# Kernel tuning notes

Measured on AMD Instinct MI355X. Metric: run time of the kernel, lower is better.

## Reference

```python
import jax, jax.numpy as jnp
import numpy as np

N_NODES = 50000
IN_DIM = 256
HID = 128
OUT_DIM = 64
N_LAYERS = 3
N_EDGES = 800000
BATCH = 4096
BN_EPS = 1e-5
LRELU_SLOPE = 0.01


def setup_inputs() -> dict:
    key = jax.random.key(0)
    ks = jax.random.split(key, 24)
    inp = {}
    inp["x"] = jax.random.normal(ks[0], (N_NODES, IN_DIM), jnp.float32)
    inp["edge_index"] = jax.random.randint(ks[1], (2, N_EDGES), 0, N_NODES, dtype=jnp.int32)
    inp["drug_pos_ids"] = jax.random.randint(ks[2], (BATCH,), 0, N_NODES, dtype=jnp.int32)
    inp["target_pos_ids"] = jax.random.randint(ks[3], (BATCH,), 0, N_NODES, dtype=jnp.int32)
    inp["drug_neg_ids"] = jax.random.randint(ks[4], (BATCH,), 0, N_NODES, dtype=jnp.int32)
    inp["target_neg_ids"] = jax.random.randint(ks[5], (BATCH,), 0, N_NODES, dtype=jnp.int32)
    inp["adjacency_matrix"] = jnp.zeros((1, 1), jnp.float32)  # dead arg in original forward
    # GCN layer params (xavier-normal-ish scale, zero bias as in __init__)
    for i in range(N_LAYERS):
        din = IN_DIM if i == 0 else HID
        inp[f"gcn_w{i}"] = jax.random.normal(ks[6 + i], (HID, din), jnp.float32) * np.float32(np.sqrt(2.0 / (din + HID)))
        inp[f"gcn_b{i}"] = jnp.zeros((HID,), jnp.float32)
    inp["bn_gamma"] = jnp.ones((HID,), jnp.float32)
    inp["bn_beta"] = jnp.zeros((HID,), jnp.float32)
    inp["W_D"] = jax.random.normal(ks[10], (HID, HID), jnp.float32) * np.float32(np.sqrt(2.0 / HID))
    inp["W_T"] = jax.random.normal(ks[11], (HID, HID), jnp.float32) * np.float32(np.sqrt(2.0 / HID))
    inp["q_D"] = jax.random.normal(ks[12], (HID,), jnp.float32)
    inp["q_T"] = jax.random.normal(ks[13], (HID,), jnp.float32)
    inp["out_w"] = jax.random.normal(ks[14], (OUT_DIM, HID), jnp.float32) * np.float32(np.sqrt(1.0 / HID))
    inp["out_b"] = jnp.zeros((OUT_DIM,), jnp.float32)
    return inp


def gcn_conv(x, w, b, src, dst, num_nodes):
    # PyG GCNConv: h = x @ W^T, then symmetric-normalized aggregation with self-loops
    h = x @ w.T                                           # [N, HID]
    deg = 1.0 + jax.ops.segment_sum(jnp.ones(src.shape[0], h.dtype), dst, num_segments=num_nodes)
    dinv = jax.lax.rsqrt(deg)                             # [N]
    norm = dinv[src] * dinv[dst]                          # [E]
    agg = jax.ops.segment_sum(h[src] * norm[:, None], dst, num_segments=num_nodes)
    agg = agg + h * (dinv * dinv)[:, None]                # self-loop contribution
    return agg + b


def batchnorm(x, gamma, beta):
    # training-mode BatchNorm1d math (batch statistics, biased var)
    mean = jnp.mean(x, axis=0)
    var = jnp.mean(jnp.square(x - mean), axis=0)
    return (x - mean) * jax.lax.rsqrt(var + BN_EPS) * gamma + beta


def attention_pooling(emb, W, q):
    # emb: [L, N, H]; softmax over the layer axis L
    h = jax.nn.leaky_relu(jnp.einsum('lnh,kh->lnk', emb, W), negative_slope=LRELU_SLOPE)
    e = jnp.einsum('lnk,k->ln', h, q)                     # [L, N]
    alpha = jax.nn.softmax(e, axis=0)
    return jnp.einsum('lnh,ln->nh', emb, alpha)           # [N, H]


def reference(x, edge_index, drug_pos_ids, target_pos_ids, drug_neg_ids, target_neg_ids,
              adjacency_matrix, gcn_w0, gcn_b0, gcn_w1, gcn_b1, gcn_w2, gcn_b2,
              bn_gamma, bn_beta, W_D, W_T, q_D, q_T, out_w, out_b):
    src, dst = edge_index[0], edge_index[1]
    num_nodes = x.shape[0]
    gcn_params = [(gcn_w0, gcn_b0), (gcn_w1, gcn_b1), (gcn_w2, gcn_b2)]
    layer_embs = []
    h = x
    for w, b in gcn_params:
        h = jax.nn.relu(gcn_conv(h, w, b, src, dst, num_nodes))
        h = batchnorm(h, bn_gamma, bn_beta)
        # dropout: identity (eval mode)
        layer_embs.append(h)
    emb = jnp.stack(layer_embs, axis=0)                   # [L, N, H]
    z_D = attention_pooling(emb, W_D, q_D) @ out_w.T + out_b
    z_T = attention_pooling(emb, W_T, q_T) @ out_w.T + out_b
    return (z_D[drug_pos_ids], z_T[target_pos_ids], z_D[drug_neg_ids], z_T[target_neg_ids])
```

## Files before the change

### kernel.cpp

```cpp
#include <hip/hip_runtime.h>
#include <hip/hip_fp16.h>
#include <cstdint>

#define N_NODES 50000
#define IN_DIM  256
#define HID     128
#define OUT_DIM 64
#define N_EDGES 800000
#define BATCH   4096
#define BN_EPS  1e-5f
#define SLOPE   0.01f

typedef unsigned short u16;
typedef __attribute__((ext_vector_type(8))) short bf16x8;
typedef __attribute__((ext_vector_type(4))) float f32x4;

__device__ __forceinline__ u16 f2bf(float f) {
    union { float f; unsigned u; } v; v.f = f;
    unsigned r = v.u + 0x7FFF + ((v.u >> 16) & 1);
    return (u16)(r >> 16);
}
__device__ __forceinline__ float bf2f(u16 b) {
    union { unsigned u; float f; } v; v.u = ((unsigned)b) << 16;
    return v.f;
}
__device__ __forceinline__ void splitbf(float v, u16* hi, u16* lo) {
    u16 h = f2bf(v);
    *hi = h;
    *lo = f2bf(v - bf2f(h));
}

__device__ __forceinline__ void swz_store(u16* __restrict__ buf, int K, int n, int k, float v) {
    int KC = K >> 7;
    int chunk = (n >> 6) * KC + (k >> 7);
    int base = chunk * 16384 + ((n >> 4) & 3) * 2048 + ((k >> 5) & 3) * 512
             + (((k >> 3) & 3) * 16 + (n & 15)) * 8 + (k & 7);
    u16 hi, lo;
    splitbf(v, &hi, &lo);
    buf[base] = hi;
    buf[base + 8192] = lo;
}

#define BNP_SPREAD 64
#define BNACC_PER_LAYER (BNP_SPREAD * 256)


#define PW0 (HID * IN_DIM)
#define PW1 (PW0 + HID * HID)
#define PW2 (PW1 + HID * HID)
#define PWD (PW2 + HID * HID)
#define PWT (PWD + HID * HID)
#define POW (PWT + OUT_DIM * HID)
#define PBN (POW + 3 * BNACC_PER_LAYER)
#define PBC (PBN + 256)
#define PTOT (PBC + 2 * 3 * 2 * BATCH)

__global__ void prep(const float* __restrict__ w0, const float* __restrict__ w1,
                     const float* __restrict__ w2, const float* __restrict__ WD,
                     const float* __restrict__ WT, const float* __restrict__ out_w,
                     u16* __restrict__ w0swz, u16* __restrict__ w1swz, u16* __restrict__ w2swz,
                     u16* __restrict__ wDTswz,
                     float* __restrict__ wt, float* __restrict__ bnacc3,
                     int* __restrict__ bucketCnt, float* __restrict__ ebuf) {
    int i = blockIdx.x * 256 + threadIdx.x;
    if (i < PW0) {
        swz_store(w0swz, IN_DIM, i >> 8, i & 255, w0[i]);
    } else if (i < PW1) {
        int j = i - PW0; swz_store(w1swz, HID, j >> 7, j & 127, w1[j]);
    } else if (i < PW2) {
        int j = i - PW1; swz_store(w2swz, HID, j >> 7, j & 127, w2[j]);
    } else if (i < PWD) {
        int j = i - PW2; swz_store(wDTswz, HID, j >> 7, j & 127, WD[j]);
    } else if (i < PWT) {
        int j = i - PWD; swz_store(wDTswz + 32768, HID, j >> 7, j & 127, WT[j]);
    } else if (i < POW) {
        int j = i - PWT;
        wt[j] = out_w[(j & 63) * HID + (j >> 6)];
    } else if (i < PBN) {
        bnacc3[i - POW] = 0.f;
    } else if (i < PBC) {
        bucketCnt[i - PBN] = 0;
    } else if (i < PTOT) {
        ebuf[i - PBC] = 0.f;
    }
}


#define NBKT 196
#define PASSA_CHUNK 2048
#define NB_A ((N_EDGES + PASSA_CHUNK - 1) / PASSA_CHUNK)

__global__ void bucket_count(const int* __restrict__ dst, int* __restrict__ bucketCnt) {
    __shared__ int hist[NBKT];
    int t = threadIdx.x;
    if (t < NBKT) hist[t] = 0;
    __syncthreads();
    int b0 = blockIdx.x * PASSA_CHUNK;
    int b1 = min(b0 + PASSA_CHUNK, N_EDGES);
    for (int i = b0 + t; i < b1; i += 256)
        atomicAdd(&hist[dst[i] >> 8], 1);
    __syncthreads();
    if (t < NBKT && hist[t] > 0) atomicAdd(&bucketCnt[t], hist[t]);
}

__global__ void bucket_scan(const int* __restrict__ bucketCnt, int* __restrict__ bucketBase,
                            int* __restrict__ gcursor, int* __restrict__ rowstart) {
    __shared__ int s[256];
    int t = threadIdx.x;
    int v = (t < NBKT) ? bucketCnt[t] : 0;
    s[t] = v;
    __syncthreads();
#pragma unroll
    for (int off = 1; off < 256; off <<= 1) {
        int tmp = (t >= off) ? s[t - off] : 0;
        __syncthreads();
        s[t] += tmp;
        __syncthreads();
    }
    if (t < NBKT) { bucketBase[t] = s[t] - v; gcursor[t] = s[t] - v; }
    if (t == 0) { bucketBase[NBKT] = N_EDGES; rowstart[N_NODES] = N_EDGES; }
}

__global__ void bucket_scatter(const int* __restrict__ src, const int* __restrict__ dst,
                               int* __restrict__ gcursor, unsigned* __restrict__ pairs) {
    __shared__ int hist[NBKT], base[NBKT], hist2[NBKT];
    int t = threadIdx.x;
    if (t < NBKT) { hist[t] = 0; hist2[t] = 0; }
    __syncthreads();
    int b0 = blockIdx.x * PASSA_CHUNK;
    int b1 = min(b0 + PASSA_CHUNK, N_EDGES);
    for (int i = b0 + t; i < b1; i += 256)
        atomicAdd(&hist[dst[i] >> 8], 1);
    __syncthreads();
    if (t < NBKT && hist[t] > 0) base[t] = atomicAdd(&gcursor[t], hist[t]);
    __syncthreads();
    for (int i = b0 + t; i < b1; i += 256) {
        int d = dst[i];
        int b = d >> 8;
        int lp = atomicAdd(&hist2[b], 1);
        pairs[base[b] + lp] = ((unsigned)(d & 255) << 16) | (unsigned)src[i];
    }
}

__global__ void bucket_build(const unsigned* __restrict__ pairs, const int* __restrict__ bucketBase,
                             int* __restrict__ rowstart, float* __restrict__ dinv,
                             int* __restrict__ csr) {
    __shared__ int cnt[256], s[256], lcur[256];
    int b = blockIdx.x, t = threadIdx.x;
    int pb0 = bucketBase[b], pb1 = bucketBase[b + 1];
    cnt[t] = 0;
    __syncthreads();
    for (int i = pb0 + t; i < pb1; i += 256)
        atomicAdd(&cnt[pairs[i] >> 16], 1);
    __syncthreads();
    int v = cnt[t];
    s[t] = v;
    __syncthreads();
#pragma unroll
    for (int off = 1; off < 256; off <<= 1) {
        int tmp = (t >= off) ? s[t - off] : 0;
        __syncthreads();
        s[t] += tmp;
        __syncthreads();
    }
    int node = (b << 8) + t;
    int start = pb0 + s[t] - v;
    if (node < N_NODES) {
        rowstart[node] = start;
        dinv[node] = rsqrtf(1.0f + (float)v);
    }
    lcur[t] = start;
    __syncthreads();
    for (int i = pb0 + t; i < pb1; i += 256) {
        unsigned pr = pairs[i];
        int pos = atomicAdd(&lcur[pr >> 16], 1);
        csr[pos] = (int)(pr & 0xFFFFu);
    }
}

__global__ void csr_pack(int* __restrict__ csr, const float* __restrict__ dinv) {
    int e = blockIdx.x * 256 + threadIdx.x;
    if (e < N_EDGES) {
        int sc = csr[e];
        __half hd = __float2half(dinv[sc]);
        csr[e] = ((int)*(u16*)&hd << 16) | sc;
    }
}


__global__ __launch_bounds__(256) void gemm_tile(const float* __restrict__ A,
                                                 const float* __restrict__ bnss,
                                                 const u16* __restrict__ Bswz,
                                                 u16* __restrict__ Cout,
                                                 int M, int K) {
    __shared__ u16 Bs[32768];
    const int tid  = threadIdx.x;
    const int wave = tid >> 6, lane = tid & 63;
    const int lr   = lane & 15, quad = lane >> 4;
    const int rowBase = blockIdx.x * 64;
    const int KC = K >> 7;

    f32x4 acc[8];
#pragma unroll
    for (int c = 0; c < 8; ++c) acc[c] = (f32x4){0.f, 0.f, 0.f, 0.f};

    const int arow = rowBase + wave * 16 + lr;
    const bool rv = arow < M;

    for (int kc = 0; kc < KC; ++kc) {
        if (kc) __syncthreads();
        const uint4* s0 = (const uint4*)(Bswz + (size_t)kc * 16384);
        const uint4* s1 = (const uint4*)(Bswz + (size_t)(KC + kc) * 16384);
        uint4* B4 = (uint4*)Bs;
#pragma unroll
        for (int i = 0; i < 8; ++i)
            B4[i * 256 + tid] = s0[i * 256 + tid];
#pragma unroll
        for (int i = 0; i < 8; ++i)
            B4[2048 + i * 256 + tid] = s1[i * 256 + tid];
        __syncthreads();

#pragma unroll
        for (int kkidx = 0; kkidx < 4; ++kkidx) {
            const int kcol = kc * 128 + kkidx * 32 + quad * 8;
            float av[8];
            if (rv) {
                const float* ap = A + (size_t)arow * K + kcol;
                float4 v0 = ((const float4*)ap)[0];
                float4 v1 = ((const float4*)ap)[1];
                av[0] = v0.x; av[1] = v0.y; av[2] = v0.z; av[3] = v0.w;
                av[4] = v1.x; av[5] = v1.y; av[6] = v1.z; av[7] = v1.w;
            } else {
#pragma unroll
                for (int j = 0; j < 8; ++j) av[j] = 0.f;
            }
            if (bnss) {
#pragma unroll
                for (int j = 0; j < 8; ++j) {
                    float sc = bnss[kcol + j];
                    float sh = bnss[K + kcol + j];
                    av[j] = fmaf(av[j], sc, sh);
                }
            }
            bf16x8 ah, al;
#pragma unroll
            for (int j = 0; j < 8; ++j) {
                u16 hi, lo;
                splitbf(av[j], &hi, &lo);
                ((u16*)&ah)[j] = hi; ((u16*)&al)[j] = lo;
            }
#pragma unroll
            for (int c = 0; c < 8; ++c) {
                const int lb = (c >> 2) * 16384 + (c & 3) * 2048 + kkidx * 512 + lane * 8;
                bf16x8 bh = *(const bf16x8*)&Bs[lb];
                bf16x8 bl = *(const bf16x8*)&Bs[lb + 8192];
                acc[c] = __builtin_amdgcn_mfma_f32_16x16x32_bf16(al, bh, acc[c], 0, 0, 0);
                acc[c] = __builtin_amdgcn_mfma_f32_16x16x32_bf16(ah, bl, acc[c], 0, 0, 0);
                acc[c] = __builtin_amdgcn_mfma_f32_16x16x32_bf16(ah, bh, acc[c], 0, 0, 0);
            }
        }
    }

    const int rowb = rowBase + wave * 16 + quad * 4;
#pragma unroll
    for (int reg = 0; reg < 4; ++reg) {
        int row = rowb + reg;
        if (row < M) {
#pragma unroll
            for (int c = 0; c < 8; ++c) {
                int col = c * 16 + lr;
                __half hv = __float2half(acc[c][reg]);
                Cout[(size_t)row * 128 + col] = *(u16*)&hv;
            }
        }
    }
}


__global__ __launch_bounds__(256) void pool_gemm(const float* __restrict__ emb0,
                                                 const float* __restrict__ emb1,
                                                 const float* __restrict__ emb2,
                                                 const float* __restrict__ bnss3,
                                                 const int* __restrict__ dpos, const int* __restrict__ dneg,
                                                 const int* __restrict__ tpos, const int* __restrict__ tneg,
                                                 const u16* __restrict__ wDTswz,
                                                 const float* __restrict__ q_D, const float* __restrict__ q_T,
                                                 float* __restrict__ e_D, float* __restrict__ e_T) {
    __shared__ u16 Bs[32768];
    const int head = blockIdx.y;
    const u16* Bswz = wDTswz + head * 32768;
    const float* q  = head ? q_T : q_D;
    float* eo = head ? e_T : e_D;
    const int* ia = head ? tpos : dpos;
    const int* ib = head ? tneg : dneg;

    const int tid  = threadIdx.x;
    const int wave = tid >> 6, lane = tid & 63;
    const int lr   = lane & 15, quad = lane >> 4;
    const int rowBase = blockIdx.x * 64;

    const int arow = rowBase + wave * 16 + lr;
    const int l0 = arow >> 13, j0 = arow & 8191;
    const int node0 = (j0 < BATCH) ? ia[j0] : ib[j0 - BATCH];
    const float* embs[3] = {emb0, emb1, emb2};
    const float* A0 = embs[l0] + (size_t)node0 * HID;
    const float* bn0 = bnss3 + l0 * 2 * HID;

    f32x4 acc[8];
#pragma unroll
    for (int c = 0; c < 8; ++c) acc[c] = (f32x4){0.f, 0.f, 0.f, 0.f};

    uint4* B4 = (uint4*)Bs;
    const uint4* srcB = (const uint4*)Bswz;
#pragma unroll
    for (int i = 0; i < 16; ++i)
        B4[i * 256 + tid] = srcB[i * 256 + tid];
    __syncthreads();

#pragma unroll
    for (int kkidx = 0; kkidx < 4; ++kkidx) {
        const int kcol = kkidx * 32 + quad * 8;
        float av[8];
        {
            float4 v0 = ((const float4*)(A0 + kcol))[0];
            float4 v1 = ((const float4*)(A0 + kcol))[1];
            av[0] = v0.x; av[1] = v0.y; av[2] = v0.z; av[3] = v0.w;
            av[4] = v1.x; av[5] = v1.y; av[6] = v1.z; av[7] = v1.w;
        }
#pragma unroll
        for (int j = 0; j < 8; ++j)
            av[j] = fmaf(av[j], bn0[kcol + j], bn0[HID + kcol + j]);
        bf16x8 ah, al;
#pragma unroll
        for (int j = 0; j < 8; ++j) {
            u16 hi, lo;
            splitbf(av[j], &hi, &lo);
            ((u16*)&ah)[j] = hi; ((u16*)&al)[j] = lo;
        }
#pragma unroll
        for (int c = 0; c < 8; ++c) {
            const int lb = (c >> 2) * 16384 + (c & 3) * 2048 + kkidx * 512 + lane * 8;
            bf16x8 bh = *(const bf16x8*)&Bs[lb];
            bf16x8 bl = *(const bf16x8*)&Bs[lb + 8192];
            acc[c] = __builtin_amdgcn_mfma_f32_16x16x32_bf16(al, bh, acc[c], 0, 0, 0);
            acc[c] = __builtin_amdgcn_mfma_f32_16x16x32_bf16(ah, bl, acc[c], 0, 0, 0);
            acc[c] = __builtin_amdgcn_mfma_f32_16x16x32_bf16(ah, bh, acc[c], 0, 0, 0);
        }
    }

    float qv[8];
#pragma unroll
    for (int c = 0; c < 8; ++c) qv[c] = q[c * 16 + lr];
    const int rowb = rowBase + wave * 16 + quad * 4;
#pragma unroll
    for (int reg = 0; reg < 4; ++reg) {
        float p = 0.f;
#pragma unroll
        for (int c = 0; c < 8; ++c) {
            float v = acc[c][reg];
            v = (v > 0.f) ? v : SLOPE * v;
            p = fmaf(v, qv[c], p);
        }
        p += __shfl_xor(p, 1);
        p += __shfl_xor(p, 2);
        p += __shfl_xor(p, 4);
        p += __shfl_xor(p, 8);
        if (lr == 0) eo[rowb + reg] = p;
    }
}


__global__ __launch_bounds__(256) void agg_relu(const u16* __restrict__ h,
                                                const float* __restrict__ dinv,
                                                const int* __restrict__ rowstart,
                                                const int* __restrict__ csr,
                                                const float* __restrict__ bias,
                                                float* __restrict__ out,
                                                float* __restrict__ bnpart) {
    __shared__ float s_s[HID], s_sq[HID];
    int tid  = threadIdx.x;
    int wave = tid >> 6;
    int lane = tid & 63;
    int ep = lane >> 5;
    int q  = lane & 31;
    if (tid < HID) { s_s[tid] = 0.f; s_sq[tid] = 0.f; }
    __syncthreads();

    float bs0 = 0.f, bs1 = 0.f, bs2 = 0.f, bs3 = 0.f;
    float bq0 = 0.f, bq1 = 0.f, bq2 = 0.f, bq3 = 0.f;

#pragma unroll
    for (int it = 0; it < 4; ++it) {
        int n = blockIdx.x * 16 + wave * 4 + it;
        if (n < N_NODES) {
            int s = rowstart[n], e1 = rowstart[n + 1];
            float ax = 0.f, ay = 0.f, az = 0.f, aw = 0.f;
            int e = s + ep;
            for (; e + 6 < e1; e += 8) {
                unsigned c0 = (unsigned)csr[e];
                unsigned c1 = (unsigned)csr[e + 2];
                unsigned c2 = (unsigned)csr[e + 4];
                unsigned c3 = (unsigned)csr[e + 6];
                u16 d0 = (u16)(c0 >> 16), d1 = (u16)(c1 >> 16), d2 = (u16)(c2 >> 16), d3 = (u16)(c3 >> 16);
                float dv0 = __half2float(*(const __half*)&d0);
                float dv1 = __half2float(*(const __half*)&d1);
                float dv2 = __half2float(*(const __half*)&d2);
                float dv3 = __half2float(*(const __half*)&d3);
                uint2 w0 = ((const uint2*)(h + (size_t)(c0 & 0xFFFFu) * HID))[q];
                uint2 w1 = ((const uint2*)(h + (size_t)(c1 & 0xFFFFu) * HID))[q];
                uint2 w2 = ((const uint2*)(h + (size_t)(c2 & 0xFFFFu) * HID))[q];
                uint2 w3 = ((const uint2*)(h + (size_t)(c3 & 0xFFFFu) * HID))[q];
                float2 a0 = __half22float2(*(const __half2*)&w0.x), b0 = __half22float2(*(const __half2*)&w0.y);
                float2 a1 = __half22float2(*(const __half2*)&w1.x), b1 = __half22float2(*(const __half2*)&w1.y);
                float2 a2 = __half22float2(*(const __half2*)&w2.x), b2 = __half22float2(*(const __half2*)&w2.y);
                float2 a3 = __half22float2(*(const __half2*)&w3.x), b3 = __half22float2(*(const __half2*)&w3.y);
                ax = fmaf(dv0, a0.x, ax); ay = fmaf(dv0, a0.y, ay); az = fmaf(dv0, b0.x, az); aw = fmaf(dv0, b0.y, aw);
                ax = fmaf(dv1, a1.x, ax); ay = fmaf(dv1, a1.y, ay); az = fmaf(dv1, b1.x, az); aw = fmaf(dv1, b1.y, aw);
                ax = fmaf(dv2, a2.x, ax); ay = fmaf(dv2, a2.y, ay); az = fmaf(dv2, b2.x, az); aw = fmaf(dv2, b2.y, aw);
                ax = fmaf(dv3, a3.x, ax); ay = fmaf(dv3, a3.y, ay); az = fmaf(dv3, b3.x, az); aw = fmaf(dv3, b3.y, aw);
            }
            for (; e < e1; e += 2) {
                unsigned c0 = (unsigned)csr[e];
                u16 d0 = (u16)(c0 >> 16);
                float dv = __half2float(*(const __half*)&d0);
                uint2 w0 = ((const uint2*)(h + (size_t)(c0 & 0xFFFFu) * HID))[q];
                float2 a0 = __half22float2(*(const __half2*)&w0.x);
                float2 b0 = __half22float2(*(const __half2*)&w0.y);
                ax = fmaf(dv, a0.x, ax); ay = fmaf(dv, a0.y, ay);
                az = fmaf(dv, b0.x, az); aw = fmaf(dv, b0.y, aw);
            }
            ax += __shfl_xor(ax, 32);
            ay += __shfl_xor(ay, 32);
            az += __shfl_xor(az, 32);
            aw += __shfl_xor(aw, 32);
            if (ep == 0) {
                float dn = dinv[n];
                float dn2 = dn * dn;
                uint2 hw = ((const uint2*)(h + (size_t)n * HID))[q];
                float2 h0 = __half22float2(*(const __half2*)&hw.x);
                float2 h1 = __half22float2(*(const __half2*)&hw.y);
                float4 bv = ((const float4*)bias)[q];
                float4 o;
                o.x = fmaxf(fmaf(ax, dn, fmaf(h0.x, dn2, bv.x)), 0.f);
                o.y = fmaxf(fmaf(ay, dn, fmaf(h0.y, dn2, bv.y)), 0.f);
                o.z = fmaxf(fmaf(az, dn, fmaf(h1.x, dn2, bv.z)), 0.f);
                o.w = fmaxf(fmaf(aw, dn, fmaf(h1.y, dn2, bv.w)), 0.f);
                ((float4*)(out + (size_t)n * HID))[q] = o;
                bs0 += o.x; bq0 = fmaf(o.x, o.x, bq0);
                bs1 += o.y; bq1 = fmaf(o.y, o.y, bq1);
                bs2 += o.z; bq2 = fmaf(o.z, o.z, bq2);
                bs3 += o.w; bq3 = fmaf(o.w, o.w, bq3);
            }
        }
    }

    if (ep == 0) {
        atomicAdd(&s_s[q * 4 + 0], bs0);
        atomicAdd(&s_s[q * 4 + 1], bs1);
        atomicAdd(&s_s[q * 4 + 2], bs2);
        atomicAdd(&s_s[q * 4 + 3], bs3);
        atomicAdd(&s_sq[q * 4 + 0], bq0);
        atomicAdd(&s_sq[q * 4 + 1], bq1);
        atomicAdd(&s_sq[q * 4 + 2], bq2);
        atomicAdd(&s_sq[q * 4 + 3], bq3);
    }
    __syncthreads();
    float* bp = bnpart + (size_t)(blockIdx.x & (BNP_SPREAD - 1)) * 256;
    if (tid < HID) atomicAdd(&bp[tid], s_s[tid]);
    else           atomicAdd(&bp[tid], s_sq[tid - HID]);
}

__global__ void bn_finalize(const float* __restrict__ acc,
                            const float* __restrict__ gamma, const float* __restrict__ beta,
                            float* __restrict__ bnss) {
    int f = threadIdx.x;
    float st = 0.f, sqt = 0.f;
    for (int p = 0; p < BNP_SPREAD; ++p) {
        st  += acc[p * 256 + f];
        sqt += acc[p * 256 + HID + f];
    }
    float mean = st * (1.0f / N_NODES);
    float var  = fmaxf(sqt * (1.0f / N_NODES) - mean * mean, 0.f);
    float sc   = gamma[f] * rsqrtf(var + BN_EPS);
    bnss[f] = sc;
    bnss[HID + f] = beta[f] - mean * sc;
}


__global__ void softmax_pool(const float* __restrict__ e0, const float* __restrict__ e1,
                             const float* __restrict__ e2, const float* __restrict__ bnss3,
                             const int* __restrict__ dpos, const int* __restrict__ dneg,
                             const int* __restrict__ tpos, const int* __restrict__ tneg,
                             const float* __restrict__ e_D, const float* __restrict__ e_T,
                             float* __restrict__ P_D, float* __restrict__ P_T) {
    int j = blockIdx.x;
    int f = threadIdx.x;
    int head = blockIdx.y;
    const int* ia = head ? tpos : dpos;
    const int* ib = head ? tneg : dneg;
    const float* e = head ? e_T : e_D;
    float* P = head ? P_T : P_D;
    int node = (j < BATCH) ? ia[j] : ib[j - BATCH];
    float l0 = e[j], l1 = e[2 * BATCH + j], l2 = e[4 * BATCH + j];
    float m = fmaxf(l0, fmaxf(l1, l2));
    float a0 = expf(l0 - m), a1 = expf(l1 - m), a2 = expf(l2 - m);
    float inv = 1.0f / (a0 + a1 + a2);
    float v0 = fmaf(e0[(size_t)node * HID + f], bnss3[f],           bnss3[HID + f]);
    float v1 = fmaf(e1[(size_t)node * HID + f], bnss3[2 * HID + f], bnss3[3 * HID + f]);
    float v2 = fmaf(e2[(size_t)node * HID + f], bnss3[4 * HID + f], bnss3[5 * HID + f]);
    P[(size_t)j * HID + f] = (a0 * v0 + a1 * v1 + a2 * v2) * inv;
}


__global__ __launch_bounds__(256) void head_gemm(const float* __restrict__ P_D,
                                                 const float* __restrict__ P_T,
                                                 const float* __restrict__ B,
                                                 const float* __restrict__ bias,
                                                 float* __restrict__ out) {
    constexpr int BM = 64, BK = 32, BN = OUT_DIM, TM = 4, TN = 4;
    __shared__ float As[BK][BM];
    __shared__ float Bs[BK][BN];
    const int y = blockIdx.y;
    const float* A = ((y & 1) ? P_T : P_D) + (size_t)(y >> 1) * BATCH * HID;
    float* C = out + (size_t)y * BATCH * OUT_DIM;
    const int tid = threadIdx.x;
    const int tx = tid & 15, ty = tid >> 4;
    const int rowBase = blockIdx.x * BM;
    float acc[TM][TN];
#pragma unroll
    for (int i = 0; i < TM; ++i)
#pragma unroll
        for (int j = 0; j < TN; ++j) acc[i][j] = 0.f;

    for (int kk = 0; kk < HID; kk += BK) {
#pragma unroll
        for (int i = tid; i < (BM * BK) / 4; i += 256) {
            int m  = i >> 3;
            int kq = i & 7;
            float4 v = *(const float4*)(A + (size_t)(rowBase + m) * HID + kk + kq * 4);
            As[kq * 4 + 0][m] = v.x;
            As[kq * 4 + 1][m] = v.y;
            As[kq * 4 + 2][m] = v.z;
            As[kq * 4 + 3][m] = v.w;
        }
#pragma unroll
        for (int i = tid; i < (BK * BN) / 4; i += 256) {
            int k  = i / (BN / 4);
            int n4 = i % (BN / 4);
            *(float4*)&Bs[k][n4 * 4] = *(const float4*)(B + (size_t)(kk + k) * BN + n4 * 4);
        }
        __syncthreads();
#pragma unroll 8
        for (int k = 0; k < BK; ++k) {
            float a[TM], b[TN];
#pragma unroll
            for (int i = 0; i < TM; ++i) a[i] = As[k][ty * TM + i];
#pragma unroll
            for (int j = 0; j < TN; ++j) b[j] = Bs[k][tx * TN + j];
#pragma unroll
            for (int i = 0; i < TM; ++i)
#pragma unroll
                for (int j = 0; j < TN; ++j)
                    acc[i][j] = fmaf(a[i], b[j], acc[i][j]);
        }
        __syncthreads();
    }
#pragma unroll
    for (int i = 0; i < TM; ++i) {
        int grow = rowBase + ty * TM + i;
#pragma unroll
        for (int j = 0; j < TN; ++j)
            C[(size_t)grow * BN + tx * TN + j] = acc[i][j] + bias[tx * TN + j];
    }
}


extern "C" void kernel_launch(void* const* d_in, const int* in_sizes, int n_in,
                              void* d_out, int out_size, void* d_ws, size_t ws_size,
                              hipStream_t stream) {
    const float* x          = (const float*)d_in[0];
    const int*   ei         = (const int*)d_in[1];
    const int*   srcp       = ei;
    const int*   dstp       = ei + N_EDGES;
    const int*   drug_pos   = (const int*)d_in[2];
    const int*   target_pos = (const int*)d_in[3];
    const int*   drug_neg   = (const int*)d_in[4];
    const int*   target_neg = (const int*)d_in[5];
    const float* gcn_w[3]   = {(const float*)d_in[7], (const float*)d_in[9], (const float*)d_in[11]};
    const float* gcn_b[3]   = {(const float*)d_in[8], (const float*)d_in[10], (const float*)d_in[12]};
    const float* gamma      = (const float*)d_in[13];
    const float* beta       = (const float*)d_in[14];
    const float* W_D        = (const float*)d_in[15];
    const float* W_T        = (const float*)d_in[16];
    const float* q_D        = (const float*)d_in[17];
    const float* q_T        = (const float*)d_in[18];
    const float* out_w      = (const float*)d_in[19];
    const float* out_b      = (const float*)d_in[20];
    float*       out        = (float*)d_out;

    char* p = (char*)d_ws;
    auto alloc = [&](size_t bytes) -> char* {
        char* r = p;
        p += (bytes + 255) & ~(size_t)255;
        return r;
    };
    char*  reg1  = alloc(sizeof(float) * (size_t)N_NODES * HID);
    float* emb0  = (float*)alloc(sizeof(float) * (size_t)N_NODES * HID);
    float* emb1  = (float*)alloc(sizeof(float) * (size_t)N_NODES * HID);
    float* emb2  = (float*)alloc(sizeof(float) * (size_t)N_NODES * HID);
    float* ebuf  = (float*)alloc(sizeof(float) * (size_t)2 * 3 * 2 * BATCH);
    u16*   w0swz = (u16*)alloc(sizeof(u16) * 2 * HID * IN_DIM);
    u16*   w1swz = (u16*)alloc(sizeof(u16) * 2 * HID * HID);
    u16*   w2swz = (u16*)alloc(sizeof(u16) * 2 * HID * HID);
    u16*   wDTswz = (u16*)alloc(sizeof(u16) * 4 * HID * HID);
    float* wt    = (float*)alloc(sizeof(float) * OUT_DIM * HID);
    int*   rowstart = (int*)alloc(sizeof(int) * (N_NODES + 1));
    int*   csr   = (int*)alloc(sizeof(int) * N_EDGES);
    unsigned* pairs = (unsigned*)alloc(sizeof(unsigned) * N_EDGES);
    float* dinvp = (float*)alloc(sizeof(float) * N_NODES);
    int*   bucketCnt  = (int*)alloc(sizeof(int) * 256);
    int*   bucketBase = (int*)alloc(sizeof(int) * (NBKT + 1));
    int*   gcursor    = (int*)alloc(sizeof(int) * 256);
    float* bnacc3 = (float*)alloc(sizeof(float) * 3 * BNACC_PER_LAYER);
    float* bnss3  = (float*)alloc(sizeof(float) * 3 * 2 * HID);
    if ((size_t)(p - (char*)d_ws) > ws_size) return;

    u16*   hbuf = (u16*)reg1;
    float* P_D  = (float*)reg1;
    float* P_T  = P_D + (size_t)2 * BATCH * HID;
    float* e_D  = ebuf;
    float* e_T  = ebuf + 3 * 2 * BATCH;
    float* embp[3] = {emb0, emb1, emb2};
    const u16* wswz[3] = {w0swz, w1swz, w2swz};

    prep<<<(PTOT + 255) / 256, 256, 0, stream>>>(
        gcn_w[0], gcn_w[1], gcn_w[2], W_D, W_T, out_w,
        w0swz, w1swz, w2swz, wDTswz, wt, bnacc3, bucketCnt, ebuf);

    bucket_count<<<NB_A, 256, 0, stream>>>(dstp, bucketCnt);
    bucket_scan<<<1, 256, 0, stream>>>(bucketCnt, bucketBase, gcursor, rowstart);
    bucket_scatter<<<NB_A, 256, 0, stream>>>(srcp, dstp, gcursor, pairs);
    bucket_build<<<NBKT, 256, 0, stream>>>(pairs, bucketBase, rowstart, dinvp, csr);
    csr_pack<<<(N_EDGES + 255) / 256, 256, 0, stream>>>(csr, dinvp);

    const int GB = (N_NODES + 63) / 64;
    for (int l = 0; l < 3; ++l) {
        int din = (l == 0) ? IN_DIM : HID;
        const float* Ain = (l == 0) ? x : embp[l - 1];
        const float* bnss = (l == 0) ? nullptr : (bnss3 + (l - 1) * 2 * HID);
        gemm_tile<<<GB, 256, 0, stream>>>(Ain, bnss, wswz[l], hbuf, N_NODES, din);
        agg_relu<<<(N_NODES + 15) / 16, 256, 0, stream>>>(hbuf, dinvp, rowstart, csr, gcn_b[l],
                                                          embp[l], bnacc3 + l * BNACC_PER_LAYER);
        bn_finalize<<<1, HID, 0, stream>>>(bnacc3 + l * BNACC_PER_LAYER, gamma, beta,
                                           bnss3 + l * 2 * HID);
    }

    const int RG = 3 * 2 * BATCH;
    pool_gemm<<<dim3(RG / 64, 2), 256, 0, stream>>>(
        emb0, emb1, emb2, bnss3, drug_pos, drug_neg, target_pos, target_neg,
        wDTswz, q_D, q_T, e_D, e_T);
    softmax_pool<<<dim3(2 * BATCH, 2), HID, 0, stream>>>(
        emb0, emb1, emb2, bnss3, drug_pos, drug_neg, target_pos, target_neg,
        e_D, e_T, P_D, P_T);

    head_gemm<<<dim3(BATCH / 64, 4), 256, 0, stream>>>(P_D, P_T, wt, out_b, out);
}
```

Before: 412.7 us.

## Map four nodes per wave with 16 lanes each using 16-byte row gathers

Result: faster. 403.9 us (-2.1%).

```diff
diff --git a/kernel.cpp b/kernel.cpp
--- a/kernel.cpp
+++ b/kernel.cpp
@@ -381,88 +381,130 @@
     int tid  = threadIdx.x;
     int wave = tid >> 6;
     int lane = tid & 63;
-    int ep = lane >> 5;
-    int q  = lane & 31;
+    int slot = lane >> 4;
+    int q    = lane & 15;
     if (tid < HID) { s_s[tid] = 0.f; s_sq[tid] = 0.f; }
     __syncthreads();
 
-    float bs0 = 0.f, bs1 = 0.f, bs2 = 0.f, bs3 = 0.f;
-    float bq0 = 0.f, bq1 = 0.f, bq2 = 0.f, bq3 = 0.f;
-
-#pragma unroll
-    for (int it = 0; it < 4; ++it) {
-        int n = blockIdx.x * 16 + wave * 4 + it;
-        if (n < N_NODES) {
-            int s = rowstart[n], e1 = rowstart[n + 1];
-            float ax = 0.f, ay = 0.f, az = 0.f, aw = 0.f;
-            int e = s + ep;
-            for (; e + 6 < e1; e += 8) {
-                unsigned c0 = (unsigned)csr[e];
-                unsigned c1 = (unsigned)csr[e + 2];
-                unsigned c2 = (unsigned)csr[e + 4];
-                unsigned c3 = (unsigned)csr[e + 6];
-                u16 d0 = (u16)(c0 >> 16), d1 = (u16)(c1 >> 16), d2 = (u16)(c2 >> 16), d3 = (u16)(c3 >> 16);
-                float dv0 = __half2float(*(const __half*)&d0);
-                float dv1 = __half2float(*(const __half*)&d1);
-                float dv2 = __half2float(*(const __half*)&d2);
-                float dv3 = __half2float(*(const __half*)&d3);
-                uint2 w0 = ((const uint2*)(h + (size_t)(c0 & 0xFFFFu) * HID))[q];
-                uint2 w1 = ((const uint2*)(h + (size_t)(c1 & 0xFFFFu) * HID))[q];
-                uint2 w2 = ((const uint2*)(h + (size_t)(c2 & 0xFFFFu) * HID))[q];
-                uint2 w3 = ((const uint2*)(h + (size_t)(c3 & 0xFFFFu) * HID))[q];
-                float2 a0 = __half22float2(*(const __half2*)&w0.x), b0 = __half22float2(*(const __half2*)&w0.y);
-                float2 a1 = __half22float2(*(const __half2*)&w1.x), b1 = __half22float2(*(const __half2*)&w1.y);
-                float2 a2 = __half22float2(*(const __half2*)&w2.x), b2 = __half22float2(*(const __half2*)&w2.y);
-                float2 a3 = __half22float2(*(const __half2*)&w3.x), b3 = __half22float2(*(const __half2*)&w3.y);
-                ax = fmaf(dv0, a0.x, ax); ay = fmaf(dv0, a0.y, ay); az = fmaf(dv0, b0.x, az); aw = fmaf(dv0, b0.y, aw);
-                ax = fmaf(dv1, a1.x, ax); ay = fmaf(dv1, a1.y, ay); az = fmaf(dv1, b1.x, az); aw = fmaf(dv1, b1.y, aw);
-                ax = fmaf(dv2, a2.x, ax); ay = fmaf(dv2, a2.y, ay); az = fmaf(dv2, b2.x, az); aw = fmaf(dv2, b2.y, aw);
-                ax = fmaf(dv3, a3.x, ax); ay = fmaf(dv3, a3.y, ay); az = fmaf(dv3, b3.x, az); aw = fmaf(dv3, b3.y, aw);
-            }
-            for (; e < e1; e += 2) {
-                unsigned c0 = (unsigned)csr[e];
-                u16 d0 = (u16)(c0 >> 16);
-                float dv = __half2float(*(const __half*)&d0);
-                uint2 w0 = ((const uint2*)(h + (size_t)(c0 & 0xFFFFu) * HID))[q];
-                float2 a0 = __half22float2(*(const __half2*)&w0.x);
-                float2 b0 = __half22float2(*(const __half2*)&w0.y);
-                ax = fmaf(dv, a0.x, ax); ay = fmaf(dv, a0.y, ay);
-                az = fmaf(dv, b0.x, az); aw = fmaf(dv, b0.y, aw);
-            }
-            ax += __shfl_xor(ax, 32);
-            ay += __shfl_xor(ay, 32);
-            az += __shfl_xor(az, 32);
-            aw += __shfl_xor(aw, 32);
-            if (ep == 0) {
-                float dn = dinv[n];
-                float dn2 = dn * dn;
-                uint2 hw = ((const uint2*)(h + (size_t)n * HID))[q];
-                float2 h0 = __half22float2(*(const __half2*)&hw.x);
-                float2 h1 = __half22float2(*(const __half2*)&hw.y);
-                float4 bv = ((const float4*)bias)[q];
-                float4 o;
-                o.x = fmaxf(fmaf(ax, dn, fmaf(h0.x, dn2, bv.x)), 0.f);
-                o.y = fmaxf(fmaf(ay, dn, fmaf(h0.y, dn2, bv.y)), 0.f);
-                o.z = fmaxf(fmaf(az, dn, fmaf(h1.x, dn2, bv.z)), 0.f);
-                o.w = fmaxf(fmaf(aw, dn, fmaf(h1.y, dn2, bv.w)), 0.f);
-                ((float4*)(out + (size_t)n * HID))[q] = o;
-                bs0 += o.x; bq0 = fmaf(o.x, o.x, bq0);
-                bs1 += o.y; bq1 = fmaf(o.y, o.y, bq1);
-                bs2 += o.z; bq2 = fmaf(o.z, o.z, bq2);
-                bs3 += o.w; bq3 = fmaf(o.w, o.w, bq3);
-            }
-        }
-    }
-
-    if (ep == 0) {
-        atomicAdd(&s_s[q * 4 + 0], bs0);
-        atomicAdd(&s_s[q * 4 + 1], bs1);
-        atomicAdd(&s_s[q * 4 + 2], bs2);
-        atomicAdd(&s_s[q * 4 + 3], bs3);
-        atomicAdd(&s_sq[q * 4 + 0], bq0);
-        atomicAdd(&s_sq[q * 4 + 1], bq1);
-        atomicAdd(&s_sq[q * 4 + 2], bq2);
-        atomicAdd(&s_sq[q * 4 + 3], bq3);
+    float bs[8], bq[8];
+#pragma unroll
+    for (int j = 0; j < 8; ++j) { bs[j] = 0.f; bq[j] = 0.f; }
+
+    int n = blockIdx.x * 16 + wave * 4 + slot;
+    if (n < N_NODES) {
+        int s = rowstart[n], e1 = rowstart[n + 1];
+        float a[8];
+#pragma unroll
+        for (int j = 0; j < 8; ++j) a[j] = 0.f;
+
+        int e = s;
+        for (; e + 3 < e1; e += 4) {
+            unsigned c0 = (unsigned)csr[e];
+            unsigned c1 = (unsigned)csr[e + 1];
+            unsigned c2 = (unsigned)csr[e + 2];
+            unsigned c3 = (unsigned)csr[e + 3];
+            u16 d0 = (u16)(c0 >> 16), d1 = (u16)(c1 >> 16), d2 = (u16)(c2 >> 16), d3 = (u16)(c3 >> 16);
+            float dv0 = __half2float(*(const __half*)&d0);
+            float dv1 = __half2float(*(const __half*)&d1);
+            float dv2 = __half2float(*(const __half*)&d2);
+            float dv3 = __half2float(*(const __half*)&d3);
+            uint4 w0 = ((const uint4*)(h + (size_t)(c0 & 0xFFFFu) * HID))[q];
+            uint4 w1 = ((const uint4*)(h + (size_t)(c1 & 0xFFFFu) * HID))[q];
+            uint4 w2 = ((const uint4*)(h + (size_t)(c2 & 0xFFFFu) * HID))[q];
+            uint4 w3 = ((const uint4*)(h + (size_t)(c3 & 0xFFFFu) * HID))[q];
+            {
+                float2 p0 = __half22float2(*(const __half2*)&w0.x);
+                float2 p1 = __half22float2(*(const __half2*)&w0.y);
+                float2 p2 = __half22float2(*(const __half2*)&w0.z);
+                float2 p3 = __half22float2(*(const __half2*)&w0.w);
+                a[0] = fmaf(dv0, p0.x, a[0]); a[1] = fmaf(dv0, p0.y, a[1]);
+                a[2] = fmaf(dv0, p1.x, a[2]); a[3] = fmaf(dv0, p1.y, a[3]);
+                a[4] = fmaf(dv0, p2.x, a[4]); a[5] = fmaf(dv0, p2.y, a[5]);
+                a[6] = fmaf(dv0, p3.x, a[6]); a[7] = fmaf(dv0, p3.y, a[7]);
+            }
+            {
+                float2 p0 = __half22float2(*(const __half2*)&w1.x);
+                float2 p1 = __half22float2(*(const __half2*)&w1.y);
+                float2 p2 = __half22float2(*(const __half2*)&w1.z);
+                float2 p3 = __half22float2(*(const __half2*)&w1.w);
+                a[0] = fmaf(dv1, p0.x, a[0]); a[1] = fmaf(dv1, p0.y, a[1]);
+                a[2] = fmaf(dv1, p1.x, a[2]); a[3] = fmaf(dv1, p1.y, a[3]);
+                a[4] = fmaf(dv1, p2.x, a[4]); a[5] = fmaf(dv1, p2.y, a[5]);
+                a[6] = fmaf(dv1, p3.x, a[6]); a[7] = fmaf(dv1, p3.y, a[7]);
+            }
+            {
+                float2 p0 = __half22float2(*(const __half2*)&w2.x);
+                float2 p1 = __half22float2(*(const __half2*)&w2.y);
+                float2 p2 = __half22float2(*(const __half2*)&w2.z);
+                float2 p3 = __half22float2(*(const __half2*)&w2.w);
+                a[0] = fmaf(dv2, p0.x, a[0]); a[1] = fmaf(dv2, p0.y, a[1]);
+                a[2] = fmaf(dv2, p1.x, a[2]); a[3] = fmaf(dv2, p1.y, a[3]);
+                a[4] = fmaf(dv2, p2.x, a[4]); a[5] = fmaf(dv2, p2.y, a[5]);
+                a[6] = fmaf(dv2, p3.x, a[6]); a[7] = fmaf(dv2, p3.y, a[7]);
+            }
+            {
+                float2 p0 = __half22float2(*(const __half2*)&w3.x);
+                float2 p1 = __half22float2(*(const __half2*)&w3.y);
+                float2 p2 = __half22float2(*(const __half2*)&w3.z);
+                float2 p3 = __half22float2(*(const __half2*)&w3.w);
+                a[0] = fmaf(dv3, p0.x, a[0]); a[1] = fmaf(dv3, p0.y, a[1]);
+                a[2] = fmaf(dv3, p1.x, a[2]); a[3] = fmaf(dv3, p1.y, a[3]);
+                a[4] = fmaf(dv3, p2.x, a[4]); a[5] = fmaf(dv3, p2.y, a[5]);
+                a[6] = fmaf(dv3, p3.x, a[6]); a[7] = fmaf(dv3, p3.y, a[7]);
+            }
+        }
+        for (; e < e1; ++e) {
+            unsigned c0 = (unsigned)csr[e];
+            u16 d0 = (u16)(c0 >> 16);
+            float dv0 = __half2float(*(const __half*)&d0);
+            uint4 w0 = ((const uint4*)(h + (size_t)(c0 & 0xFFFFu) * HID))[q];
+            float2 p0 = __half22float2(*(const __half2*)&w0.x);
+            float2 p1 = __half22float2(*(const __half2*)&w0.y);
+            float2 p2 = __half22float2(*(const __half2*)&w0.z);
+            float2 p3 = __half22float2(*(const __half2*)&w0.w);
+            a[0] = fmaf(dv0, p0.x, a[0]); a[1] = fmaf(dv0, p0.y, a[1]);
+            a[2] = fmaf(dv0, p1.x, a[2]); a[3] = fmaf(dv0, p1.y, a[3]);
+            a[4] = fmaf(dv0, p2.x, a[4]); a[5] = fmaf(dv0, p2.y, a[5]);
+            a[6] = fmaf(dv0, p3.x, a[6]); a[7] = fmaf(dv0, p3.y, a[7]);
+        }
+
+        float dn = dinv[n];
+        float dn2 = dn * dn;
+        uint4 hw = ((const uint4*)(h + (size_t)n * HID))[q];
+        float2 h0 = __half22float2(*(const __half2*)&hw.x);
+        float2 h1 = __half22float2(*(const __half2*)&hw.y);
+        float2 h2 = __half22float2(*(const __half2*)&hw.z);
+        float2 h3 = __half22float2(*(const __half2*)&hw.w);
+        float hv[8] = {h0.x, h0.y, h1.x, h1.y, h2.x, h2.y, h3.x, h3.y};
+        float4 bv0 = ((const float4*)bias)[2 * q];
+        float4 bv1 = ((const float4*)bias)[2 * q + 1];
+        float bb[8] = {bv0.x, bv0.y, bv0.z, bv0.w, bv1.x, bv1.y, bv1.z, bv1.w};
+        float o[8];
+#pragma unroll
+        for (int j = 0; j < 8; ++j) {
+            o[j] = fmaxf(fmaf(a[j], dn, fmaf(hv[j], dn2, bb[j])), 0.f);
+            bs[j] += o[j];
+            bq[j] = fmaf(o[j], o[j], bq[j]);
+        }
+        float4 o0 = {o[0], o[1], o[2], o[3]};
+        float4 o1 = {o[4], o[5], o[6], o[7]};
+        ((float4*)(out + (size_t)n * HID))[2 * q]     = o0;
+        ((float4*)(out + (size_t)n * HID))[2 * q + 1] = o1;
+    }
+
+#pragma unroll
+    for (int j = 0; j < 8; ++j) {
+        bs[j] += __shfl_xor(bs[j], 16);
+        bs[j] += __shfl_xor(bs[j], 32);
+        bq[j] += __shfl_xor(bq[j], 16);
+        bq[j] += __shfl_xor(bq[j], 32);
+    }
+    if (slot == 0) {
+#pragma unroll
+        for (int j = 0; j < 8; ++j) {
+            atomicAdd(&s_s[q * 8 + j], bs[j]);
+            atomicAdd(&s_sq[q * 8 + j], bq[j]);
+        }
     }
     __syncthreads();
     float* bp = bnpart + (size_t)(blockIdx.x & (BNP_SPREAD - 1)) * 256;
```

## Pre-scale GEMM rows by dinv, slice features into 32-wide blocks for aggregation

Applied to the files above, without the earlier changes.

Result: slower. 472.3 us (+14.4%).

```diff
diff --git a/kernel.cpp b/kernel.cpp
--- a/kernel.cpp
+++ b/kernel.cpp
@@ -144,7 +144,7 @@
 
 __global__ void bucket_build(const unsigned* __restrict__ pairs, const int* __restrict__ bucketBase,
                              int* __restrict__ rowstart, float* __restrict__ dinv,
-                             int* __restrict__ csr) {
+                             u16* __restrict__ csr) {
     __shared__ int cnt[256], s[256], lcur[256];
     int b = blockIdx.x, t = threadIdx.x;
     int pb0 = bucketBase[b], pb1 = bucketBase[b + 1];
@@ -174,16 +174,7 @@
     for (int i = pb0 + t; i < pb1; i += 256) {
         unsigned pr = pairs[i];
         int pos = atomicAdd(&lcur[pr >> 16], 1);
-        csr[pos] = (int)(pr & 0xFFFFu);
-    }
-}
-
-__global__ void csr_pack(int* __restrict__ csr, const float* __restrict__ dinv) {
-    int e = blockIdx.x * 256 + threadIdx.x;
-    if (e < N_EDGES) {
-        int sc = csr[e];
-        __half hd = __float2half(dinv[sc]);
-        csr[e] = ((int)*(u16*)&hd << 16) | sc;
+        csr[pos] = (u16)(pr & 0xFFFFu);
     }
 }
 
@@ -191,6 +182,7 @@
 __global__ __launch_bounds__(256) void gemm_tile(const float* __restrict__ A,
                                                  const float* __restrict__ bnss,
                                                  const u16* __restrict__ Bswz,
+                                                 const float* __restrict__ dinv,
                                                  u16* __restrict__ Cout,
                                                  int M, int K) {
     __shared__ u16 Bs[32768];
@@ -266,11 +258,13 @@
     for (int reg = 0; reg < 4; ++reg) {
         int row = rowb + reg;
         if (row < M) {
+            float dn = dinv[row];
 #pragma unroll
             for (int c = 0; c < 8; ++c) {
-                int col = c * 16 + lr;
-                __half hv = __float2half(acc[c][reg]);
-                Cout[(size_t)row * 128 + col] = *(u16*)&hv;
+                __half hv = __float2half(acc[c][reg] * dn);
+                u16* dst = Cout + (size_t)(c >> 1) * ((size_t)N_NODES * 32)
+                         + (size_t)row * 32 + (c & 1) * 16 + lr;
+                __builtin_nontemporal_store(*(u16*)&hv, dst);
             }
         }
     }
@@ -370,104 +364,79 @@
 }
 
 
-__global__ __launch_bounds__(256) void agg_relu(const u16* __restrict__ h,
-                                                const float* __restrict__ dinv,
-                                                const int* __restrict__ rowstart,
-                                                const int* __restrict__ csr,
-                                                const float* __restrict__ bias,
-                                                float* __restrict__ out,
-                                                float* __restrict__ bnpart) {
-    __shared__ float s_s[HID], s_sq[HID];
-    int tid  = threadIdx.x;
-    int wave = tid >> 6;
-    int lane = tid & 63;
-    int ep = lane >> 5;
-    int q  = lane & 31;
-    if (tid < HID) { s_s[tid] = 0.f; s_sq[tid] = 0.f; }
-    __syncthreads();
-
-    float bs0 = 0.f, bs1 = 0.f, bs2 = 0.f, bs3 = 0.f;
-    float bq0 = 0.f, bq1 = 0.f, bq2 = 0.f, bq3 = 0.f;
-
-#pragma unroll
-    for (int it = 0; it < 4; ++it) {
-        int n = blockIdx.x * 16 + wave * 4 + it;
-        if (n < N_NODES) {
-            int s = rowstart[n], e1 = rowstart[n + 1];
-            float ax = 0.f, ay = 0.f, az = 0.f, aw = 0.f;
-            int e = s + ep;
-            for (; e + 6 < e1; e += 8) {
-                unsigned c0 = (unsigned)csr[e];
-                unsigned c1 = (unsigned)csr[e + 2];
-                unsigned c2 = (unsigned)csr[e + 4];
-                unsigned c3 = (unsigned)csr[e + 6];
-                u16 d0 = (u16)(c0 >> 16), d1 = (u16)(c1 >> 16), d2 = (u16)(c2 >> 16), d3 = (u16)(c3 >> 16);
-                float dv0 = __half2float(*(const __half*)&d0);
-                float dv1 = __half2float(*(const __half*)&d1);
-                float dv2 = __half2float(*(const __half*)&d2);
-                float dv3 = __half2float(*(const __half*)&d3);
-                uint2 w0 = ((const uint2*)(h + (size_t)(c0 & 0xFFFFu) * HID))[q];
-                uint2 w1 = ((const uint2*)(h + (size_t)(c1 & 0xFFFFu) * HID))[q];
-                uint2 w2 = ((const uint2*)(h + (size_t)(c2 & 0xFFFFu) * HID))[q];
-                uint2 w3 = ((const uint2*)(h + (size_t)(c3 & 0xFFFFu) * HID))[q];
-                float2 a0 = __half22float2(*(const __half2*)&w0.x), b0 = __half22float2(*(const __half2*)&w0.y);
-                float2 a1 = __half22float2(*(const __half2*)&w1.x), b1 = __half22float2(*(const __half2*)&w1.y);
-                float2 a2 = __half22float2(*(const __half2*)&w2.x), b2 = __half22float2(*(const __half2*)&w2.y);
-                float2 a3 = __half22float2(*(const __half2*)&w3.x), b3 = __half22float2(*(const __half2*)&w3.y);
-                ax = fmaf(dv0, a0.x, ax); ay = fmaf(dv0, a0.y, ay); az = fmaf(dv0, b0.x, az); aw = fmaf(dv0, b0.y, aw);
-                ax = fmaf(dv1, a1.x, ax); ay = fmaf(dv1, a1.y, ay); az = fmaf(dv1, b1.x, az); aw = fmaf(dv1, b1.y, aw);
-                ax = fmaf(dv2, a2.x, ax); ay = fmaf(dv2, a2.y, ay); az = fmaf(dv2, b2.x, az); aw = fmaf(dv2, b2.y, aw);
-                ax = fmaf(dv3, a3.x, ax); ay = fmaf(dv3, a3.y, ay); az = fmaf(dv3, b3.x, az); aw = fmaf(dv3, b3.y, aw);
-            }
-            for (; e < e1; e += 2) {
-                unsigned c0 = (unsigned)csr[e];
-                u16 d0 = (u16)(c0 >> 16);
-                float dv = __half2float(*(const __half*)&d0);
-                uint2 w0 = ((const uint2*)(h + (size_t)(c0 & 0xFFFFu) * HID))[q];
-                float2 a0 = __half22float2(*(const __half2*)&w0.x);
-                float2 b0 = __half22float2(*(const __half2*)&w0.y);
-                ax = fmaf(dv, a0.x, ax); ay = fmaf(dv, a0.y, ay);
-                az = fmaf(dv, b0.x, az); aw = fmaf(dv, b0.y, aw);
-            }
-            ax += __shfl_xor(ax, 32);
-            ay += __shfl_xor(ay, 32);
-            az += __shfl_xor(az, 32);
-            aw += __shfl_xor(aw, 32);
-            if (ep == 0) {
-                float dn = dinv[n];
-                float dn2 = dn * dn;
-                uint2 hw = ((const uint2*)(h + (size_t)n * HID))[q];
-                float2 h0 = __half22float2(*(const __half2*)&hw.x);
-                float2 h1 = __half22float2(*(const __half2*)&hw.y);
-                float4 bv = ((const float4*)bias)[q];
-                float4 o;
-                o.x = fmaxf(fmaf(ax, dn, fmaf(h0.x, dn2, bv.x)), 0.f);
-                o.y = fmaxf(fmaf(ay, dn, fmaf(h0.y, dn2, bv.y)), 0.f);
-                o.z = fmaxf(fmaf(az, dn, fmaf(h1.x, dn2, bv.z)), 0.f);
-                o.w = fmaxf(fmaf(aw, dn, fmaf(h1.y, dn2, bv.w)), 0.f);
-                ((float4*)(out + (size_t)n * HID))[q] = o;
-                bs0 += o.x; bq0 = fmaf(o.x, o.x, bq0);
-                bs1 += o.y; bq1 = fmaf(o.y, o.y, bq1);
-                bs2 += o.z; bq2 = fmaf(o.z, o.z, bq2);
-                bs3 += o.w; bq3 = fmaf(o.w, o.w, bq3);
-            }
-        }
-    }
-
-    if (ep == 0) {
-        atomicAdd(&s_s[q * 4 + 0], bs0);
-        atomicAdd(&s_s[q * 4 + 1], bs1);
-        atomicAdd(&s_s[q * 4 + 2], bs2);
-        atomicAdd(&s_s[q * 4 + 3], bs3);
-        atomicAdd(&s_sq[q * 4 + 0], bq0);
-        atomicAdd(&s_sq[q * 4 + 1], bq1);
-        atomicAdd(&s_sq[q * 4 + 2], bq2);
-        atomicAdd(&s_sq[q * 4 + 3], bq3);
+#define AGG_NG ((N_NODES + 127) / 128)
+
+__global__ __launch_bounds__(256) void agg_slice(const u16* __restrict__ hblk,
+                                                 const float* __restrict__ dinv,
+                                                 const int* __restrict__ rowstart,
+                                                 const u16* __restrict__ csr,
+                                                 const float* __restrict__ bias,
+                                                 float* __restrict__ out,
+                                                 float* __restrict__ bnpart) {
+    __shared__ float s_s[32], s_sq[32];
+    const int tid  = threadIdx.x;
+    const int wave = tid >> 6, lane = tid & 63;
+    const int eg = lane >> 3;
+    const int q  = lane & 7;
+    const int x = blockIdx.x & 7;
+    const int slice = x >> 1, sub = x & 1;
+    const int g = blockIdx.x >> 3;
+    const u16* hs = hblk + (size_t)slice * ((size_t)N_NODES * 32);
+    if (tid < 32) { s_s[tid] = 0.f; s_sq[tid] = 0.f; }
+    __syncthreads();
+
+    float bsum[4] = {0.f, 0.f, 0.f, 0.f}, bsq[4] = {0.f, 0.f, 0.f, 0.f};
+    const int nbase = ((g * 2 + sub) * 4 + wave) * 16;
+    float4 bv = ((const float4*)(bias + slice * 32))[q];
+
+    for (int it = 0; it < 16; ++it) {
+        int n = nbase + it;
+        if (n >= N_NODES) break;
+        int s = rowstart[n], e1 = rowstart[n + 1];
+        float dn = dinv[n];
+        float a0 = 0.f, a1 = 0.f, a2 = 0.f, a3 = 0.f;
+#pragma unroll 2
+        for (int e = s + eg; e < e1; e += 8) {
+            int c = csr[e];
+            uint2 w = *(const uint2*)(hs + (size_t)c * 32 + q * 4);
+            float2 p0 = __half22float2(*(const __half2*)&w.x);
+            float2 p1 = __half22float2(*(const __half2*)&w.y);
+            a0 += p0.x; a1 += p0.y; a2 += p1.x; a3 += p1.y;
+        }
+        a0 += __shfl_xor(a0, 8);  a1 += __shfl_xor(a1, 8);
+        a2 += __shfl_xor(a2, 8);  a3 += __shfl_xor(a3, 8);
+        a0 += __shfl_xor(a0, 16); a1 += __shfl_xor(a1, 16);
+        a2 += __shfl_xor(a2, 16); a3 += __shfl_xor(a3, 16);
+        a0 += __shfl_xor(a0, 32); a1 += __shfl_xor(a1, 32);
+        a2 += __shfl_xor(a2, 32); a3 += __shfl_xor(a3, 32);
+        if (eg == 0) {
+            uint2 sw = *(const uint2*)(hs + (size_t)n * 32 + q * 4);
+            float2 s0 = __half22float2(*(const __half2*)&sw.x);
+            float2 s1 = __half22float2(*(const __half2*)&sw.y);
+            f32x4 o;
+            o.x = fmaxf(fmaf(dn, a0 + s0.x, bv.x), 0.f);
+            o.y = fmaxf(fmaf(dn, a1 + s0.y, bv.y), 0.f);
+            o.z = fmaxf(fmaf(dn, a2 + s1.x, bv.z), 0.f);
+            o.w = fmaxf(fmaf(dn, a3 + s1.y, bv.w), 0.f);
+            __builtin_nontemporal_store(o, (f32x4*)(out + (size_t)n * HID + slice * 32 + q * 4));
+            bsum[0] += o.x; bsq[0] = fmaf(o.x, o.x, bsq[0]);
+            bsum[1] += o.y; bsq[1] = fmaf(o.y, o.y, bsq[1]);
+            bsum[2] += o.z; bsq[2] = fmaf(o.z, o.z, bsq[2]);
+            bsum[3] += o.w; bsq[3] = fmaf(o.w, o.w, bsq[3]);
+        }
+    }
+
+    if (eg == 0) {
+#pragma unroll
+        for (int j = 0; j < 4; ++j) {
+            atomicAdd(&s_s[q * 4 + j], bsum[j]);
+            atomicAdd(&s_sq[q * 4 + j], bsq[j]);
+        }
     }
     __syncthreads();
     float* bp = bnpart + (size_t)(blockIdx.x & (BNP_SPREAD - 1)) * 256;
-    if (tid < HID) atomicAdd(&bp[tid], s_s[tid]);
-    else           atomicAdd(&bp[tid], s_sq[tid - HID]);
+    if (tid < 32)      atomicAdd(&bp[slice * 32 + tid], s_s[tid]);
+    else if (tid < 64) atomicAdd(&bp[128 + slice * 32 + (tid - 32)], s_sq[tid - 32]);
 }
 
 __global__ void bn_finalize(const float* __restrict__ acc,
@@ -615,7 +584,7 @@
     u16*   wDTswz = (u16*)alloc(sizeof(u16) * 4 * HID * HID);
     float* wt    = (float*)alloc(sizeof(float) * OUT_DIM * HID);
     int*   rowstart = (int*)alloc(sizeof(int) * (N_NODES + 1));
-    int*   csr   = (int*)alloc(sizeof(int) * N_EDGES);
+    u16*   csr   = (u16*)alloc(sizeof(int) * N_EDGES);
     unsigned* pairs = (unsigned*)alloc(sizeof(unsigned) * N_EDGES);
     float* dinvp = (float*)alloc(sizeof(float) * N_NODES);
     int*   bucketCnt  = (int*)alloc(sizeof(int) * 256);
@@ -641,16 +610,15 @@
     bucket_scan<<<1, 256, 0, stream>>>(bucketCnt, bucketBase, gcursor, rowstart);
     bucket_scatter<<<NB_A, 256, 0, stream>>>(srcp, dstp, gcursor, pairs);
     bucket_build<<<NBKT, 256, 0, stream>>>(pairs, bucketBase, rowstart, dinvp, csr);
-    csr_pack<<<(N_EDGES + 255) / 256, 256, 0, stream>>>(csr, dinvp);
 
     const int GB = (N_NODES + 63) / 64;
     for (int l = 0; l < 3; ++l) {
         int din = (l == 0) ? IN_DIM : HID;
         const float* Ain = (l == 0) ? x : embp[l - 1];
         const float* bnss = (l == 0) ? nullptr : (bnss3 + (l - 1) * 2 * HID);
-        gemm_tile<<<GB, 256, 0, stream>>>(Ain, bnss, wswz[l], hbuf, N_NODES, din);
-        agg_relu<<<(N_NODES + 15) / 16, 256, 0, stream>>>(hbuf, dinvp, rowstart, csr, gcn_b[l],
-                                                          embp[l], bnacc3 + l * BNACC_PER_LAYER);
+        gemm_tile<<<GB, 256, 0, stream>>>(Ain, bnss, wswz[l], dinvp, hbuf, N_NODES, din);
+        agg_slice<<<AGG_NG * 8, 256, 0, stream>>>(hbuf, dinvp, rowstart, csr, gcn_b[l],
+                                                  embp[l], bnacc3 + l * BNACC_PER_LAYER);
         bn_finalize<<<1, HID, 0, stream>>>(bnacc3 + l * BNACC_PER_LAYER, gamma, beta,
                                            bnss3 + l * 2 * HID);
     }
```
